# Kernel optimization log

Measured on AMD Instinct MI355X. Metric: run time of the kernel, lower is better.

## Reference

```python
import jax, jax.numpy as jnp
import numpy as np

# Constants from the torch module
S_DECAY = 0.95    # sentence_decay
P_DECAY = 0.99    # paragraph_decay
D_DECAY = 0.999   # document_decay
ALPHA = 0.1       # delta_update alpha for sentence/paragraph
DOC_ALPHA = 0.05  # delta_update alpha for document
BETA = 1.0
PARA_GROUP = 5    # sentences per paragraph
EPS = 1e-12       # F.normalize eps


def _normalize(x):
    # matches torch.nn.functional.normalize(x, dim=-1)
    return x / jnp.maximum(jnp.linalg.norm(x, axis=-1, keepdims=True), EPS)


def _delta_step(M, kn, v, alpha, beta):
    # M: [H, dk, dv]; kn: [dk] (already L2-normalized); v: [dv]
    # M_new = M @ (I - alpha * kn kn^T) + beta * kn v^T   (erase matrix is symmetric,
    # so the einsum 'hkv,hkj->hjv' form equals this rank-1 update -- no dk x dk matrix needed)
    kTM = jnp.einsum('k,hkv->hv', kn, M)                       # [H, dv]
    return M - alpha * kn[None, :, None] * kTM[:, None, :] \
             + beta * (kn[:, None] * v[None, :])[None, :, :]


def _scan_updates(M0, K, V, decay, alpha, beta):
    # Streaming delta-rule: per step, decay then erase/write.
    def step(M, kv):
        k, v = kv
        M = M * decay
        M = _delta_step(M, _normalize(k), v, alpha, beta)
        return M, None
    M, _ = jax.lax.scan(step, M0, (K, V))
    return M


def setup_inputs() -> dict:
    key = jax.random.key(0)
    ks = jax.random.split(key, 7)
    T, d_emb, d_k, d_v, H = 1000, 768, 256, 256, 8
    emb = jax.random.normal(ks[0], (T, d_emb), dtype=jnp.float32)
    q = jax.random.normal(ks[1], (d_k,), dtype=jnp.float32)
    W_k = jax.random.normal(ks[2], (d_emb, d_k), dtype=jnp.float32) * 0.02
    b_k = jax.random.normal(ks[3], (d_k,), dtype=jnp.float32) * 0.02
    W_v = jax.random.normal(ks[4], (d_emb, d_v), dtype=jnp.float32) * 0.02
    b_v = jax.random.normal(ks[5], (d_v,), dtype=jnp.float32) * 0.02
    M_sent0 = jnp.zeros((H, d_k, d_v), dtype=jnp.float32)
    M_para0 = jnp.zeros((H, d_k, d_v), dtype=jnp.float32)
    M_doc0 = jnp.zeros((H, d_k, d_v), dtype=jnp.float32)
    return {"emb": emb, "q": q, "W_k": W_k, "b_k": b_k, "W_v": W_v, "b_v": b_v,
            "M_sent0": M_sent0, "M_para0": M_para0, "M_doc0": M_doc0}


def reference(emb, q, W_k, b_k, W_v, b_v, M_sent0, M_para0, M_doc0):
    T, d_emb = emb.shape
    # Level 1: sentence memory -- one delta update per sentence embedding
    K = emb @ W_k + b_k            # [T, dk]
    V = emb @ W_v + b_v            # [T, dv]
    M_sent = _scan_updates(M_sent0, K, V, S_DECAY, ALPHA, BETA)
    # Level 2: paragraph memory -- mean of each group of 5 sentence embeddings
    para_emb = emb.reshape(T // PARA_GROUP, PARA_GROUP, d_emb).mean(axis=1)
    PK = para_emb @ W_k + b_k
    PV = para_emb @ W_v + b_v
    M_para = _scan_updates(M_para0, PK, PV, P_DECAY, ALPHA, BETA)
    # Level 3: document memory -- single update from paragraph-memory statistics
    doc_k = M_para.mean(axis=0).mean(axis=-1)   # [dk]
    doc_v = M_para.mean(axis=0).mean(axis=0)    # [dv]
    M_doc = M_doc0 * D_DECAY
    M_doc = _delta_step(M_doc, _normalize(doc_k), doc_v, DOC_ALPHA, BETA)
    # recall(q, level='all')
    qn = _normalize(q)
    def recall(M):
        return jnp.einsum('hkv,k->hv', M, qn).mean(axis=0)   # [dv]
    return 0.2 * recall(M_sent) + 0.3 * recall(M_para) + 0.5 * recall(M_doc)
```

## Files before the change

kernel.cpp:

```cpp
#include <hip/hip_runtime.h>
#include <hip/hip_bf16.h>

#define ALPHA   0.1f
#define S_DECAY 0.95f
#define P_DECAY 0.99f
#define D_EMB   768
#define DK      256

template<int ctrl, int row_mask>
__device__ __forceinline__ float dpp_add(float x) {
    int y = __builtin_amdgcn_update_dpp(0, __float_as_int(x), ctrl, row_mask, 0xF, true);
    return x + __int_as_float(y);
}

template<int N>
__device__ __forceinline__ void wave_allred_arr(float (&x)[N]) {
#pragma unroll
    for (int n = 0; n < N; ++n) x[n] = dpp_add<0xB1,  0xF>(x[n]);
#pragma unroll
    for (int n = 0; n < N; ++n) x[n] = dpp_add<0x4E,  0xF>(x[n]);
#pragma unroll
    for (int n = 0; n < N; ++n) x[n] = dpp_add<0x141, 0xF>(x[n]);
#pragma unroll
    for (int n = 0; n < N; ++n) x[n] = dpp_add<0x140, 0xF>(x[n]);
#pragma unroll
    for (int n = 0; n < N; ++n) x[n] = dpp_add<0x142, 0xA>(x[n]);
#pragma unroll
    for (int n = 0; n < N; ++n) x[n] = dpp_add<0x143, 0xC>(x[n]);
#pragma unroll
    for (int n = 0; n < N; ++n)
        x[n] = __int_as_float(__builtin_amdgcn_readlane(__float_as_int(x[n]), 63));
}

__device__ __forceinline__ float dot4v(const float4& a, const float4& b) {
    float t0 = a.x * b.x; t0 = fmaf(a.y, b.y, t0);
    float t1 = a.z * b.z; t1 = fmaf(a.w, b.w, t1);
    return t0 + t1;
}

__device__ __forceinline__ float rl(float x, int lane) {
    return __int_as_float(__builtin_amdgcn_readlane(__float_as_int(x), lane));
}

__global__ __launch_bounds__(256) void prep_kernel(
    const float* __restrict__ emb,
    const float* __restrict__ Wk, const float* __restrict__ bk,
    const float* __restrict__ Wv, const float* __restrict__ bv,
    float* __restrict__ K, float* __restrict__ V, float* __restrict__ USrev,
    float* __restrict__ out, int T)
{
    const int tid = threadIdx.x;
    const int bid = blockIdx.x;
    const int NBLK = (T / 4) * 2;
    if (bid >= NBLK) {
        const int PADS = ((T + 63) / 64) * 64;
        for (int i = tid; i < (PADS - T) * DK; i += 256) USrev[(size_t)T * DK + i] = 0.f;
        out[tid] = 0.f;
        return;
    }
    const int mat = bid & 1;
    const int r0  = (bid >> 1) * 4;

    __shared__ float se[4][D_EMB];
    __shared__ float s_red[4][4];

    const float4* emb4 = reinterpret_cast<const float4*>(emb);
#pragma unroll
    for (int r = 0; r < 4; ++r) {
        if (tid < D_EMB / 4)
            reinterpret_cast<float4*>(se[r])[tid] = emb4[(size_t)(r0 + r) * (D_EMB / 4) + tid];
    }
    __syncthreads();

    const float* Wp = mat ? Wv : Wk;
    const float* bp = mat ? bv : bk;
    const int j = tid;

    float a0 = 0.f, a1 = 0.f, a2 = 0.f, a3 = 0.f;
    float c0 = Wp[j],        c1 = Wp[j + DK],     c2 = Wp[j + 2*DK], c3 = Wp[j + 3*DK];
    float p0 = Wp[j + 4*DK], p1 = Wp[j + 5*DK],   p2 = Wp[j + 6*DK], p3 = Wp[j + 7*DK];

    for (int d = 0; d < D_EMB; d += 4) {
        int dn = d + 8; if (dn >= D_EMB) dn = 0;
        const float* wn = Wp + (size_t)dn * DK + j;
        float n0 = wn[0], n1 = wn[DK], n2 = wn[2*DK], n3 = wn[3*DK];

        float4 e0 = *reinterpret_cast<const float4*>(&se[0][d]);
        float4 e1 = *reinterpret_cast<const float4*>(&se[1][d]);
        float4 e2 = *reinterpret_cast<const float4*>(&se[2][d]);
        float4 e3 = *reinterpret_cast<const float4*>(&se[3][d]);

        a0 = fmaf(e0.x, c0, a0); a0 = fmaf(e0.y, c1, a0);
        a0 = fmaf(e0.z, c2, a0); a0 = fmaf(e0.w, c3, a0);
        a1 = fmaf(e1.x, c0, a1); a1 = fmaf(e1.y, c1, a1);
        a1 = fmaf(e1.z, c2, a1); a1 = fmaf(e1.w, c3, a1);
        a2 = fmaf(e2.x, c0, a2); a2 = fmaf(e2.y, c1, a2);
        a2 = fmaf(e2.z, c2, a2); a2 = fmaf(e2.w, c3, a2);
        a3 = fmaf(e3.x, c0, a3); a3 = fmaf(e3.y, c1, a3);
        a3 = fmaf(e3.z, c2, a3); a3 = fmaf(e3.w, c3, a3);

        c0 = p0; c1 = p1; c2 = p2; c3 = p3;
        p0 = n0; p1 = n1; p2 = n2; p3 = n3;
    }

    float bj = bp[j];
    float o0 = a0 + bj, o1 = a1 + bj, o2 = a2 + bj, o3 = a3 + bj;
    float* dst = mat ? V : K;
    dst[(size_t)(r0 + 0) * DK + j] = o0;
    dst[(size_t)(r0 + 1) * DK + j] = o1;
    dst[(size_t)(r0 + 2) * DK + j] = o2;
    dst[(size_t)(r0 + 3) * DK + j] = o3;

    if (mat == 0) {
        const int wave = tid >> 6, l = tid & 63;
        float red[4] = { o0*o0, o1*o1, o2*o2, o3*o3 };
        wave_allred_arr(red);
        if (l == 0) {
            s_red[wave][0] = red[0]; s_red[wave][1] = red[1];
            s_red[wave][2] = red[2]; s_red[wave][3] = red[3];
        }
        __syncthreads();
        float t0 = s_red[0][0] + s_red[1][0] + s_red[2][0] + s_red[3][0];
        float t1 = s_red[0][1] + s_red[1][1] + s_red[2][1] + s_red[3][1];
        float t2 = s_red[0][2] + s_red[1][2] + s_red[2][2] + s_red[3][2];
        float t3 = s_red[0][3] + s_red[1][3] + s_red[2][3] + s_red[3][3];
        USrev[(size_t)(T - 1 - (r0 + 0)) * DK + j] = o0 * (1.0f / fmaxf(sqrtf(t0), 1e-12f));
        USrev[(size_t)(T - 1 - (r0 + 1)) * DK + j] = o1 * (1.0f / fmaxf(sqrtf(t1), 1e-12f));
        USrev[(size_t)(T - 1 - (r0 + 2)) * DK + j] = o2 * (1.0f / fmaxf(sqrtf(t2), 1e-12f));
        USrev[(size_t)(T - 1 - (r0 + 3)) * DK + j] = o3 * (1.0f / fmaxf(sqrtf(t3), 1e-12f));
    }
}

#define SU_STRIDE 260
__global__ __launch_bounds__(512) void mid_kernel(
    const float* __restrict__ K, const float* __restrict__ V,
    const float* __restrict__ USrev,
    float* __restrict__ UPrev, float* __restrict__ UPfwd,
    float* __restrict__ PV, float* __restrict__ SVv,
    float* __restrict__ AinvT, float* __restrict__ F1, float* __restrict__ biasF,
    int P, int NCS, int NCP)
{
    __shared__ __align__(16) float sU[64 * SU_STRIDE];
    __shared__ __align__(16) float sA[64 * 65];
    __shared__ float s_pd[64];
    __shared__ float s_sv[64];
    __shared__ float4 s_f1w[4][64];
    float* sX = sU;

    const int tid = threadIdx.x, wv = tid >> 6, l = tid & 63;
    const int bid = blockIdx.x;
    int type, m;
    if (bid < NCS)            { type = 0; m = bid; }
    else if (bid < NCS + NCP) { type = 1; m = bid - NCS; }
    else                      { type = 2; m = bid - NCS - NCP; }

    if (type == 2) {
        if (tid < 64) s_pd[tid] = powf(P_DECAY, (float)tid);
        __syncthreads();
    }

    if (type == 0) {
        const float4* U4 = reinterpret_cast<const float4*>(USrev) + (size_t)m * 4096;
        for (int idx = tid; idx < 4096; idx += 512) {
            float4 t = U4[idx];
            int row = idx >> 6, c4 = (idx & 63) << 2;
            *reinterpret_cast<float4*>(&sU[row * SU_STRIDE + c4]) = t;
        }
    } else if (type == 1) {
        if (tid < 256) {
            const float4* K4 = reinterpret_cast<const float4*>(K);
            for (int ii = 0; ii < 16; ii += 2) {
                const int iA = wv * 16 + ii, iB = iA + 1;
                const int pA = P - 1 - (64 * m + iA);
                const int pB = P - 1 - (64 * m + iB);
                float4 ka[5], kb[5];
                if (pA >= 0) {
#pragma unroll
                    for (int s = 0; s < 5; ++s) ka[s] = K4[(size_t)(5 * pA + s) * 64 + l];
                }
                if (pB >= 0) {
#pragma unroll
                    for (int s = 0; s < 5; ++s) kb[s] = K4[(size_t)(5 * pB + s) * 64 + l];
                }
                {
                    float4 u = make_float4(0.f, 0.f, 0.f, 0.f);
                    if (pA >= 0) {
                        float4 pk = make_float4(0.f, 0.f, 0.f, 0.f);
#pragma unroll
                        for (int s = 0; s < 5; ++s) {
                            pk.x += ka[s].x; pk.y += ka[s].y; pk.z += ka[s].z; pk.w += ka[s].w;
                        }
                        pk.x *= 0.2f; pk.y *= 0.2f; pk.z *= 0.2f; pk.w *= 0.2f;
                        float red[1] = { dot4v(pk, pk) };
                        wave_allred_arr(red);
                        float inv = 1.0f / fmaxf(sqrtf(red[0]), 1e-12f);
                        u = make_float4(pk.x * inv, pk.y * inv, pk.z * inv, pk.w * inv);
                    }
                    *reinterpret_cast<float4*>(&sU[iA * SU_STRIDE + 4 * l]) = u;
                    reinterpret_cast<float4*>(UPrev)[(size_t)(64 * m + iA) * 64 + l] = u;
                }
                {
                    float4 u = make_float4(0.f, 0.f, 0.f, 0.f);
                    if (pB >= 0) {
                        float4 pk = make_float4(0.f, 0.f, 0.f, 0.f);
#pragma unroll
                        for (int s = 0; s < 5; ++s) {
                            pk.x += kb[s].x; pk.y += kb[s].y; pk.z += kb[s].z; pk.w += kb[s].w;
                        }
                        pk.x *= 0.2f; pk.y *= 0.2f; pk.z *= 0.2f; pk.w *= 0.2f;
                        float red[1] = { dot4v(pk, pk) };
                        wave_allred_arr(red);
                        float inv = 1.0f / fmaxf(sqrtf(red[0]), 1e-12f);
                        u = make_float4(pk.x * inv, pk.y * inv, pk.z * inv, pk.w * inv);
                    }
                    *reinterpret_cast<float4*>(&sU[iB * SU_STRIDE + 4 * l]) = u;
                    reinterpret_cast<float4*>(UPrev)[(size_t)(64 * m + iB) * 64 + l] = u;
                }
            }
        }
    } else {
        if (tid < 256) {
            const float4* K4 = reinterpret_cast<const float4*>(K);
            const float4* V4 = reinterpret_cast<const float4*>(V);
            float4 f1p = make_float4(0.f, 0.f, 0.f, 0.f);
            for (int ii = 0; ii < 16; ii += 2) {
                const int iA = wv * 16 + ii, iB = iA + 1;
                const int pA = 64 * m + iA, pB = 64 * m + iB;
                float4 ka[5], va[5], kb[5], vb[5];
                if (pA < P) {
#pragma unroll
                    for (int s = 0; s < 5; ++s) {
                        ka[s] = K4[(size_t)(5 * pA + s) * 64 + l];
                        va[s] = V4[(size_t)(5 * pA + s) * 64 + l];
                    }
                }
                if (pB < P) {
#pragma unroll
                    for (int s = 0; s < 5; ++s) {
                        kb[s] = K4[(size_t)(5 * pB + s) * 64 + l];
                        vb[s] = V4[(size_t)(5 * pB + s) * 64 + l];
                    }
                }
                {
                    float4 u = make_float4(0.f, 0.f, 0.f, 0.f);
                    float sv = 0.f;
                    if (pA < P) {
                        float4 pk = make_float4(0.f, 0.f, 0.f, 0.f);
                        float4 pv = make_float4(0.f, 0.f, 0.f, 0.f);
#pragma unroll
                        for (int s = 0; s < 5; ++s) {
                            pk.x += ka[s].x; pk.y += ka[s].y; pk.z += ka[s].z; pk.w += ka[s].w;
                            pv.x += va[s].x; pv.y += va[s].y; pv.z += va[s].z; pv.w += va[s].w;
                        }
                        pk.x *= 0.2f; pk.y *= 0.2f; pk.z *= 0.2f; pk.w *= 0.2f;
                        pv.x *= 0.2f; pv.y *= 0.2f; pv.z *= 0.2f; pv.w *= 0.2f;
                        reinterpret_cast<float4*>(PV)[(size_t)pA * 64 + l] = pv;
                        float red[2] = { dot4v(pk, pk), pv.x + pv.y + pv.z + pv.w };
                        wave_allred_arr(red);
                        float inv = 1.0f / fmaxf(sqrtf(red[0]), 1e-12f);
                        u = make_float4(pk.x * inv, pk.y * inv, pk.z * inv, pk.w * inv);
                        sv = red[1];
                    }
                    *reinterpret_cast<float4*>(&sU[iA * SU_STRIDE + 4 * l]) = u;
                    reinterpret_cast<float4*>(UPfwd)[(size_t)(64 * m + iA) * 64 + l] = u;
                    if (l == 0) { s_sv[iA] = sv; SVv[64 * m + iA] = sv; }
                    float f = s_pd[63 - iA] * sv;
                    f1p.x = fmaf(f, u.x, f1p.x); f1p.y = fmaf(f, u.y, f1p.y);
                    f1p.z = fmaf(f, u.z, f1p.z); f1p.w = fmaf(f, u.w, f1p.w);
                }
                {
                    float4 u = make_float4(0.f, 0.f, 0.f, 0.f);
                    float sv = 0.f;
                    if (pB < P) {
                        float4 pk = make_float4(0.f, 0.f, 0.f, 0.f);
                        float4 pv = make_float4(0.f, 0.f, 0.f, 0.f);
#pragma unroll
                        for (int s = 0; s < 5; ++s) {
                            pk.x += kb[s].x; pk.y += kb[s].y; pk.z += kb[s].z; pk.w += kb[s].w;
                            pv.x += vb[s].x; pv.y += vb[s].y; pv.z += vb[s].z; pv.w += vb[s].w;
                        }
                        pk.x *= 0.2f; pk.y *= 0.2f; pk.z *= 0.2f; pk.w *= 0.2f;
                        pv.x *= 0.2f; pv.y *= 0.2f; pv.z *= 0.2f; pv.w *= 0.2f;
                        reinterpret_cast<float4*>(PV)[(size_t)pB * 64 + l] = pv;
                        float red[2] = { dot4v(pk, pk), pv.x + pv.y + pv.z + pv.w };
                        wave_allred_arr(red);
                        float inv = 1.0f / fmaxf(sqrtf(red[0]), 1e-12f);
                        u = make_float4(pk.x * inv, pk.y * inv, pk.z * inv, pk.w * inv);
                        sv = red[1];
                    }
                    *reinterpret_cast<float4*>(&sU[iB * SU_STRIDE + 4 * l]) = u;
                    reinterpret_cast<float4*>(UPfwd)[(size_t)(64 * m + iB) * 64 + l] = u;
                    if (l == 0) { s_sv[iB] = sv; SVv[64 * m + iB] = sv; }
                    float f = s_pd[63 - iB] * sv;
                    f1p.x = fmaf(f, u.x, f1p.x); f1p.y = fmaf(f, u.y, f1p.y);
                    f1p.z = fmaf(f, u.z, f1p.z); f1p.w = fmaf(f, u.w, f1p.w);
                }
            }
            s_f1w[wv][l] = f1p;
        }
    }
    __syncthreads();

    if (type == 2 && wv == 0) {
        float4 a = s_f1w[0][l], b = s_f1w[1][l], c = s_f1w[2][l], d = s_f1w[3][l];
        float4 tot = make_float4(a.x+b.x+c.x+d.x, a.y+b.y+c.y+d.y,
                                 a.z+b.z+c.z+d.z, a.w+b.w+c.w+d.w);
        reinterpret_cast<float4*>(F1)[(size_t)m * 64 + l] = tot;
    }

    {
        const int i0 = (tid & 31) * 2;
        const int j0 = (tid >> 5) * 4;
        float g[2][4];
#pragma unroll
        for (int r = 0; r < 2; ++r)
#pragma unroll
            for (int c = 0; c < 4; ++c) g[r][c] = 0.f;
#pragma unroll 4
        for (int k4 = 0; k4 < 64; ++k4) {
            float4 A0 = *reinterpret_cast<const float4*>(&sU[(i0    ) * SU_STRIDE + 4*k4]);
            float4 A1 = *reinterpret_cast<const float4*>(&sU[(i0 + 1) * SU_STRIDE + 4*k4]);
            float4 B0 = *reinterpret_cast<const float4*>(&sU[(j0    ) * SU_STRIDE + 4*k4]);
            float4 B1 = *reinterpret_cast<const float4*>(&sU[(j0 + 1) * SU_STRIDE + 4*k4]);
            float4 B2 = *reinterpret_cast<const float4*>(&sU[(j0 + 2) * SU_STRIDE + 4*k4]);
            float4 B3 = *reinterpret_cast<const float4*>(&sU[(j0 + 3) * SU_STRIDE + 4*k4]);
            g[0][0] += dot4v(A0, B0); g[0][1] += dot4v(A0, B1);
            g[0][2] += dot4v(A0, B2); g[0][3] += dot4v(A0, B3);
            g[1][0] += dot4v(A1, B0); g[1][1] += dot4v(A1, B1);
            g[1][2] += dot4v(A1, B2); g[1][3] += dot4v(A1, B3);
        }
#pragma unroll
        for (int r = 0; r < 2; ++r)
#pragma unroll
            for (int c = 0; c < 4; ++c) {
                int gi = i0 + r, gj = j0 + c;
                float val = 0.f;
                if (gj < gi) {
                    val = ALPHA * g[r][c];
                    if (type == 2) val *= s_pd[gi - gj];
                }
                sA[gi * 65 + gj] = val;
            }
    }
    __syncthreads();

    if (type == 2 && wv == 0) {
        float dotb = 0.f;
#pragma unroll
        for (int jj = 0; jj < 64; ++jj)
            dotb = fmaf(sA[l * 65 + jj], s_sv[jj], dotb);
        biasF[m * 64 + l] = dotb * (1.0f / ALPHA);
    }

    {
        const int base = (wv & 3) * 16;
        float x[16];
#pragma unroll
        for (int r = 0; r < 16; ++r) x[r] = (base + r == l && wv < 4) ? 1.f : 0.f;
        for (int s = 0; s < 4; ++s) {
            if (wv == s) {
#pragma unroll
                for (int i = 1; i < 16; ++i)
#pragma unroll
                    for (int jj = 0; jj < 16; ++jj)
                        if (jj < i)
                            x[i] = fmaf(-sA[(base + i) * 65 + (base + jj)], x[jj], x[i]);
#pragma unroll
                for (int r = 0; r < 16; ++r) sX[(base + r) * 65 + l] = x[r];
            }
            __syncthreads();
            if (wv > s && wv < 4) {
#pragma unroll
                for (int i = 0; i < 16; ++i) {
                    float xi = sX[(s * 16 + i) * 65 + l];
#pragma unroll
                    for (int r = 0; r < 16; ++r)
                        x[r] = fmaf(-sA[(base + r) * 65 + (s * 16 + i)], xi, x[r]);
                }
            }
        }
    }
    __syncthreads();

    float* dstA = AinvT + (size_t)bid * 4096;
    for (int idx = tid; idx < 4096; idx += 512) {
        int jcol = idx >> 6, irow = idx & 63;
        dstA[idx] = sX[irow * 65 + jcol];
    }
}

__global__ __launch_bounds__(512) void accum2_kernel(
    const float* __restrict__ V, const float* __restrict__ PV,
    const float* __restrict__ USrev, const float* __restrict__ UPrev,
    const float* __restrict__ UPfwd, const float* __restrict__ AinvT,
    const float* __restrict__ F1, const float* __restrict__ biasF,
    const float* __restrict__ q,
    float* __restrict__ out, int T, int P, int NCS, int NCP)
{
    __shared__ float s_cp[8][64];
    __shared__ float4 s_part[8][64];
    __shared__ float s_powd[65];
    __shared__ float s_b[64];
    __shared__ float s_cpa[4][64];
    __shared__ float wc[64];
    __shared__ float s_gs[1];

    const int b = blockIdx.x, tid = threadIdx.x;
    const int wave = tid >> 6, l = tid & 63, wb = wave * 8;

    if (tid <= 64) s_powd[tid] = powf(P_DECAY, (float)tid);

    float4 q4 = reinterpret_cast<const float4*>(q)[l];
    float qs[1] = { dot4v(q4, q4) };
    wave_allred_arr(qs);
    float qinv = 1.0f / fmaxf(sqrtf(qs[0]), 1e-12f);
    float4 qn = make_float4(q4.x * qinv, q4.y * qinv, q4.z * qinv, q4.w * qinv);
    __syncthreads();

    int ci, chunk, realN; const float* src; float decay;
    if (b < NCS)              { ci = b;             chunk = b;        src = V;  decay = S_DECAY; realN = T; }
    else if (b < NCS + NCP)   { ci = b - NCS;       chunk = NCS + ci; src = PV; decay = P_DECAY; realN = P; }
    else                      { ci = b - NCS - NCP; chunk = NCS + ci; src = PV; decay = P_DECAY; realN = P; }

    {
        const float4* U4; const float* Xb; float4 w1;
        if (b < NCS) {
            U4 = reinterpret_cast<const float4*>(USrev); Xb = AinvT; w1 = qn;
        } else if (b < NCS + NCP) {
            U4 = reinterpret_cast<const float4*>(UPrev); Xb = AinvT + (size_t)NCS * 4096; w1 = qn;
        } else {
            U4 = reinterpret_cast<const float4*>(UPrev); Xb = AinvT + (size_t)NCS * 4096;
            w1 = make_float4(1.f, 1.f, 1.f, 1.f);
        }
        for (int m = 0; m <= ci; ++m) {
            float4 curU[8];
#pragma unroll
            for (int r = 0; r < 8; ++r)
                curU[r] = U4[(size_t)m * 4096 + (size_t)(wb + r) * 64 + l];
            float d[8];
#pragma unroll
            for (int r = 0; r < 8; ++r) d[r] = dot4v(curU[r], w1);
            wave_allred_arr(d);
            if (m == ci) {
                if (l == 0) {
#pragma unroll
                    for (int r = 0; r < 8; ++r) s_b[wb + r] = d[r];
                }
                break;
            }
            float curX[8];
#pragma unroll
            for (int r = 0; r < 8; ++r)
                curX[r] = Xb[(size_t)m * 4096 + (size_t)(wb + r) * 64 + l];
            float cp = 0.f;
#pragma unroll
            for (int r = 0; r < 8; ++r) cp = fmaf(curX[r], d[r], cp);
            s_cp[wave][l] = cp;
            __syncthreads();
            float cl = 0.f;
#pragma unroll
            for (int w = 0; w < 8; ++w) cl += s_cp[w][l];
            float4 part = make_float4(0.f, 0.f, 0.f, 0.f);
#pragma unroll
            for (int r = 0; r < 8; ++r) {
                float cw = rl(cl, wb + r);
                part.x = fmaf(cw, curU[r].x, part.x); part.y = fmaf(cw, curU[r].y, part.y);
                part.z = fmaf(cw, curU[r].z, part.z); part.w = fmaf(cw, curU[r].w, part.w);
            }
            s_part[wave][l] = part;
            __syncthreads();
            float4 s = make_float4(0.f, 0.f, 0.f, 0.f);
#pragma unroll
            for (int w = 0; w < 8; ++w) {
                float4 p = s_part[w][l];
                s.x += p.x; s.y += p.y; s.z += p.z; s.w += p.w;
            }
            w1.x = fmaf(-ALPHA, s.x, w1.x); w1.y = fmaf(-ALPHA, s.y, w1.y);
            w1.z = fmaf(-ALPHA, s.z, w1.z); w1.w = fmaf(-ALPHA, s.w, w1.w);
        }
    }
    __syncthreads();

    if (b >= NCS + NCP) {
        float4 y = make_float4(0.f, 0.f, 0.f, 0.f);
        const float4* Uf4 = reinterpret_cast<const float4*>(UPfwd);
        for (int mm = 0; mm < NCP; ++mm) {
            float4 cU[8]; float cX[8];
#pragma unroll
            for (int r = 0; r < 8; ++r) {
                cU[r] = Uf4[(size_t)mm * 4096 + (size_t)(wb + r) * 64 + l];
                cX[r] = AinvT[(size_t)(NCS + NCP + mm) * 4096 + (size_t)(wb + r) * 64 + l];
            }
            float biasr[8];
#pragma unroll
            for (int r = 0; r < 8; ++r) biasr[r] = biasF[mm * 64 + wb + r];
            float4 f1 = reinterpret_cast<const float4*>(F1)[(size_t)mm * 64 + l];
            float d[8];
#pragma unroll
            for (int r = 0; r < 8; ++r) d[r] = dot4v(cU[r], y);
            wave_allred_arr(d);
#pragma unroll
            for (int r = 0; r < 8; ++r)
                d[r] = fmaf(s_powd[wb + r + 1], d[r], biasr[r]);
            float cp = 0.f;
#pragma unroll
            for (int r = 0; r < 8; ++r) cp = fmaf(cX[r], d[r], cp);
            s_cp[wave][l] = cp;
            __syncthreads();
            float cl = 0.f;
#pragma unroll
            for (int w = 0; w < 8; ++w) cl += s_cp[w][l];
            float4 part = make_float4(0.f, 0.f, 0.f, 0.f);
#pragma unroll
            for (int r = 0; r < 8; ++r) {
                float cw = s_powd[63 - (wb + r)] * rl(cl, wb + r);
                part.x = fmaf(cw, cU[r].x, part.x); part.y = fmaf(cw, cU[r].y, part.y);
                part.z = fmaf(cw, cU[r].z, part.z); part.w = fmaf(cw, cU[r].w, part.w);
            }
            s_part[wave][l] = part;
            __syncthreads();
            float4 s = make_float4(0.f, 0.f, 0.f, 0.f);
#pragma unroll
            for (int w = 0; w < 8; ++w) {
                float4 p = s_part[w][l];
                s.x += p.x; s.y += p.y; s.z += p.z; s.w += p.w;
            }
            float d64 = s_powd[64];
            y.x = fmaf(d64, y.x, fmaf(-ALPHA, s.x, f1.x));
            y.y = fmaf(d64, y.y, fmaf(-ALPHA, s.y, f1.y));
            y.z = fmaf(d64, y.z, fmaf(-ALPHA, s.z, f1.z));
            y.w = fmaf(d64, y.w, fmaf(-ALPHA, s.w, f1.w));
        }
        float fin[2] = { dot4v(y, y), dot4v(qn, y) };
        wave_allred_arr(fin);
        if (tid == 0) s_gs[0] = fin[1] / fmaxf(sqrtf(fin[0]), 2.56e-10f);
        __syncthreads();
    }

    if (tid < 256) {
        const int part = tid >> 6, k = tid & 63;
        const float* Xc = AinvT + (size_t)chunk * 4096;
        float cp = 0.f;
#pragma unroll
        for (int jj = 0; jj < 16; ++jj) {
            int j = part * 16 + jj;
            cp = fmaf(Xc[j * 64 + k], s_b[j], cp);
        }
        s_cpa[part][k] = cp;
    }
    __syncthreads();
    if (tid < 64) {
        float c = s_cpa[0][tid] + s_cpa[1][tid] + s_cpa[2][tid] + s_cpa[3][tid];
        wc[tid] = powf(decay, (float)(ci * 64 + tid)) * c;
    }
    __syncthreads();
    if (tid < 256) {
        const int k = tid;
        float acc = 0.f;
        for (int ii = 0; ii < 64; ++ii) {
            int i = ci * 64 + ii;
            if (i < realN)
                acc = fmaf(wc[ii], src[(size_t)(realN - 1 - i) * DK + k], acc);
        }
        float wlev;
        if (b < NCS)            wlev = 0.2f;
        else if (b < NCS + NCP) wlev = 0.3f;
        else                    wlev = (0.5f / 256.0f) * s_gs[0];
        atomicAdd(&out[k], wlev * acc);
    }
}

extern "C" void kernel_launch(void* const* d_in, const int* in_sizes, int n_in,
                              void* d_out, int out_size, void* d_ws, size_t ws_size,
                              hipStream_t stream) {
    const float* emb = (const float*)d_in[0];
    const float* q   = (const float*)d_in[1];
    const float* Wk  = (const float*)d_in[2];
    const float* bk  = (const float*)d_in[3];
    const float* Wv  = (const float*)d_in[4];
    const float* bv  = (const float*)d_in[5];

    const int T = in_sizes[0] / D_EMB;
    const int P = T / 5;
    const int NCS  = (T + 63) / 64;
    const int NCP  = (P + 63) / 64;
    const int PADS = NCS * 64;
    const int PADP = NCP * 64;
    const int NCH  = NCS + 2 * NCP;

    float* ws    = (float*)d_ws;
    float* K     = ws;
    float* V     = K     + (size_t)T * DK;
    float* PV    = V     + (size_t)T * DK;
    float* USrev = PV    + (size_t)PADP * DK;
    float* UPrev = USrev + (size_t)PADS * DK;
    float* UPfwd = UPrev + (size_t)PADP * DK;
    float* SVv   = UPfwd + (size_t)PADP * DK;
    float* AinvT = SVv   + PADP;
    float* F1    = AinvT + (size_t)NCH * 4096;
    float* biasF = F1    + (size_t)NCP * 256;

    prep_kernel<<<(T / 4) * 2 + 1, 256, 0, stream>>>(emb, Wk, bk, Wv, bv,
                                                     K, V, USrev, (float*)d_out, T);
    mid_kernel<<<NCH, 512, 0, stream>>>(K, V, USrev, UPrev, UPfwd, PV, SVv,
                                        AinvT, F1, biasF, P, NCS, NCP);
    accum2_kernel<<<NCH, 512, 0, stream>>>(V, PV, USrev, UPrev, UPfwd, AinvT,
                                           F1, biasF, q, (float*)d_out, T, P, NCS, NCP);
}
```

Baseline: 173.4 us.

## Run serial chunk recurrence in one wave and prefetch source rows into LDS

The sequential per-chunk recurrence in accum2_kernel now runs entirely inside wave 0, which handles all 64 rows itself and so needs no block-wide barriers per chunk. Meanwhile waves 4-7 stage the block's 64x256 source rows into a 64KB shared buffer, and threads 0-255 prefetch their AinvT slice into registers. The aim is to remove two __syncthreads per iteration and overlap the final accumulation's global loads with the serial phase. The cost is 8x more serial work per wave, heavy register pressure from the 64-entry dfull arrays, and lower occupancy from the large LDS allocation.

New measurement: 305.0 us. 75.9% more time.

```diff
diff --git a/kernel.cpp b/kernel.cpp
--- a/kernel.cpp
+++ b/kernel.cpp
@@ -397,8 +397,7 @@
     const float* __restrict__ q,
     float* __restrict__ out, int T, int P, int NCS, int NCP)
 {
-    __shared__ float s_cp[8][64];
-    __shared__ float4 s_part[8][64];
+    __shared__ float s_src[64 * 256];
     __shared__ float s_powd[65];
     __shared__ float s_b[64];
     __shared__ float s_cpa[4][64];
@@ -406,7 +405,7 @@
     __shared__ float s_gs[1];
 
     const int b = blockIdx.x, tid = threadIdx.x;
-    const int wave = tid >> 6, l = tid & 63, wb = wave * 8;
+    const int wave = tid >> 6, l = tid & 63;
 
     if (tid <= 64) s_powd[tid] = powf(P_DECAY, (float)tid);
 
@@ -422,129 +421,167 @@
     else if (b < NCS + NCP)   { ci = b - NCS;       chunk = NCS + ci; src = PV; decay = P_DECAY; realN = P; }
     else                      { ci = b - NCS - NCP; chunk = NCS + ci; src = PV; decay = P_DECAY; realN = P; }
 
-    {
-        const float4* U4; const float* Xb; float4 w1;
-        if (b < NCS) {
-            U4 = reinterpret_cast<const float4*>(USrev); Xb = AinvT; w1 = qn;
-        } else if (b < NCS + NCP) {
-            U4 = reinterpret_cast<const float4*>(UPrev); Xb = AinvT + (size_t)NCS * 4096; w1 = qn;
-        } else {
-            U4 = reinterpret_cast<const float4*>(UPrev); Xb = AinvT + (size_t)NCS * 4096;
-            w1 = make_float4(1.f, 1.f, 1.f, 1.f);
-        }
-        for (int m = 0; m <= ci; ++m) {
-            float4 curU[8];
-#pragma unroll
-            for (int r = 0; r < 8; ++r)
-                curU[r] = U4[(size_t)m * 4096 + (size_t)(wb + r) * 64 + l];
-            float d[8];
-#pragma unroll
-            for (int r = 0; r < 8; ++r) d[r] = dot4v(curU[r], w1);
-            wave_allred_arr(d);
-            if (m == ci) {
-                if (l == 0) {
-#pragma unroll
-                    for (int r = 0; r < 8; ++r) s_b[wb + r] = d[r];
-                }
-                break;
-            }
-            float curX[8];
-#pragma unroll
-            for (int r = 0; r < 8; ++r)
-                curX[r] = Xb[(size_t)m * 4096 + (size_t)(wb + r) * 64 + l];
-            float cp = 0.f;
-#pragma unroll
-            for (int r = 0; r < 8; ++r) cp = fmaf(curX[r], d[r], cp);
-            s_cp[wave][l] = cp;
-            __syncthreads();
-            float cl = 0.f;
-#pragma unroll
-            for (int w = 0; w < 8; ++w) cl += s_cp[w][l];
-            float4 part = make_float4(0.f, 0.f, 0.f, 0.f);
-#pragma unroll
-            for (int r = 0; r < 8; ++r) {
-                float cw = rl(cl, wb + r);
-                part.x = fmaf(cw, curU[r].x, part.x); part.y = fmaf(cw, curU[r].y, part.y);
-                part.z = fmaf(cw, curU[r].z, part.z); part.w = fmaf(cw, curU[r].w, part.w);
-            }
-            s_part[wave][l] = part;
-            __syncthreads();
-            float4 s = make_float4(0.f, 0.f, 0.f, 0.f);
-#pragma unroll
-            for (int w = 0; w < 8; ++w) {
-                float4 p = s_part[w][l];
-                s.x += p.x; s.y += p.y; s.z += p.z; s.w += p.w;
-            }
-            w1.x = fmaf(-ALPHA, s.x, w1.x); w1.y = fmaf(-ALPHA, s.y, w1.y);
-            w1.z = fmaf(-ALPHA, s.z, w1.z); w1.w = fmaf(-ALPHA, s.w, w1.w);
-        }
-    }
-    __syncthreads();
-
-    if (b >= NCS + NCP) {
-        float4 y = make_float4(0.f, 0.f, 0.f, 0.f);
-        const float4* Uf4 = reinterpret_cast<const float4*>(UPfwd);
-        for (int mm = 0; mm < NCP; ++mm) {
-            float4 cU[8]; float cX[8];
-#pragma unroll
-            for (int r = 0; r < 8; ++r) {
-                cU[r] = Uf4[(size_t)mm * 4096 + (size_t)(wb + r) * 64 + l];
-                cX[r] = AinvT[(size_t)(NCS + NCP + mm) * 4096 + (size_t)(wb + r) * 64 + l];
-            }
-            float biasr[8];
-#pragma unroll
-            for (int r = 0; r < 8; ++r) biasr[r] = biasF[mm * 64 + wb + r];
-            float4 f1 = reinterpret_cast<const float4*>(F1)[(size_t)mm * 64 + l];
-            float d[8];
-#pragma unroll
-            for (int r = 0; r < 8; ++r) d[r] = dot4v(cU[r], y);
-            wave_allred_arr(d);
-#pragma unroll
-            for (int r = 0; r < 8; ++r)
-                d[r] = fmaf(s_powd[wb + r + 1], d[r], biasr[r]);
-            float cp = 0.f;
-#pragma unroll
-            for (int r = 0; r < 8; ++r) cp = fmaf(cX[r], d[r], cp);
-            s_cp[wave][l] = cp;
-            __syncthreads();
-            float cl = 0.f;
-#pragma unroll
-            for (int w = 0; w < 8; ++w) cl += s_cp[w][l];
-            float4 part = make_float4(0.f, 0.f, 0.f, 0.f);
-#pragma unroll
-            for (int r = 0; r < 8; ++r) {
-                float cw = s_powd[63 - (wb + r)] * rl(cl, wb + r);
-                part.x = fmaf(cw, cU[r].x, part.x); part.y = fmaf(cw, cU[r].y, part.y);
-                part.z = fmaf(cw, cU[r].z, part.z); part.w = fmaf(cw, cU[r].w, part.w);
-            }
-            s_part[wave][l] = part;
-            __syncthreads();
-            float4 s = make_float4(0.f, 0.f, 0.f, 0.f);
-#pragma unroll
-            for (int w = 0; w < 8; ++w) {
-                float4 p = s_part[w][l];
-                s.x += p.x; s.y += p.y; s.z += p.z; s.w += p.w;
-            }
-            float d64 = s_powd[64];
-            y.x = fmaf(d64, y.x, fmaf(-ALPHA, s.x, f1.x));
-            y.y = fmaf(d64, y.y, fmaf(-ALPHA, s.y, f1.y));
-            y.z = fmaf(d64, y.z, fmaf(-ALPHA, s.z, f1.z));
-            y.w = fmaf(d64, y.w, fmaf(-ALPHA, s.w, f1.w));
-        }
-        float fin[2] = { dot4v(y, y), dot4v(qn, y) };
-        wave_allred_arr(fin);
-        if (tid == 0) s_gs[0] = fin[1] / fmaxf(sqrtf(fin[0]), 2.56e-10f);
-        __syncthreads();
-    }
-
+    float xr[16];
     if (tid < 256) {
         const int part = tid >> 6, k = tid & 63;
         const float* Xc = AinvT + (size_t)chunk * 4096;
+#pragma unroll
+        for (int jj = 0; jj < 16; ++jj)
+            xr[jj] = Xc[(part * 16 + jj) * 64 + k];
+    }
+
+    if (wave == 0) {
+        {
+            const float4* U4; const float* Xb; float4 w1;
+            if (b < NCS) {
+                U4 = reinterpret_cast<const float4*>(USrev); Xb = AinvT; w1 = qn;
+            } else if (b < NCS + NCP) {
+                U4 = reinterpret_cast<const float4*>(UPrev); Xb = AinvT + (size_t)NCS * 4096; w1 = qn;
+            } else {
+                U4 = reinterpret_cast<const float4*>(UPrev); Xb = AinvT + (size_t)NCS * 4096;
+                w1 = make_float4(1.f, 1.f, 1.f, 1.f);
+            }
+            for (int m = 0; m <= ci; ++m) {
+                const size_t base = (size_t)m * 4096;
+                float dfull[64];
+#pragma unroll
+                for (int g = 0; g < 8; ++g) {
+                    float4 u[8];
+#pragma unroll
+                    for (int r = 0; r < 8; ++r)
+                        u[r] = U4[base + (size_t)(g * 8 + r) * 64 + l];
+                    float dd[8];
+#pragma unroll
+                    for (int r = 0; r < 8; ++r) dd[r] = dot4v(u[r], w1);
+                    wave_allred_arr(dd);
+#pragma unroll
+                    for (int r = 0; r < 8; ++r) dfull[g * 8 + r] = dd[r];
+                }
+                if (m == ci) {
+                    if (l == 0) {
+#pragma unroll
+                        for (int j = 0; j < 64; ++j) s_b[j] = dfull[j];
+                    }
+                    break;
+                }
+                float cl = 0.f;
+#pragma unroll
+                for (int g = 0; g < 8; ++g) {
+                    float xg[8];
+#pragma unroll
+                    for (int r = 0; r < 8; ++r)
+                        xg[r] = Xb[base + (size_t)(g * 8 + r) * 64 + l];
+                    float cp = 0.f;
+#pragma unroll
+                    for (int r = 0; r < 8; ++r) cp = fmaf(xg[r], dfull[g * 8 + r], cp);
+                    cl += cp;
+                }
+                float4 s = make_float4(0.f, 0.f, 0.f, 0.f);
+#pragma unroll
+                for (int g = 0; g < 8; ++g) {
+                    float4 u[8];
+#pragma unroll
+                    for (int r = 0; r < 8; ++r)
+                        u[r] = U4[base + (size_t)(g * 8 + r) * 64 + l];
+                    float4 part = make_float4(0.f, 0.f, 0.f, 0.f);
+#pragma unroll
+                    for (int r = 0; r < 8; ++r) {
+                        float cw = rl(cl, g * 8 + r);
+                        part.x = fmaf(cw, u[r].x, part.x); part.y = fmaf(cw, u[r].y, part.y);
+                        part.z = fmaf(cw, u[r].z, part.z); part.w = fmaf(cw, u[r].w, part.w);
+                    }
+                    s.x += part.x; s.y += part.y; s.z += part.z; s.w += part.w;
+                }
+                w1.x = fmaf(-ALPHA, s.x, w1.x); w1.y = fmaf(-ALPHA, s.y, w1.y);
+                w1.z = fmaf(-ALPHA, s.z, w1.z); w1.w = fmaf(-ALPHA, s.w, w1.w);
+            }
+        }
+
+        if (b >= NCS + NCP) {
+            float4 y = make_float4(0.f, 0.f, 0.f, 0.f);
+            const float4* Uf4 = reinterpret_cast<const float4*>(UPfwd);
+            for (int mm = 0; mm < NCP; ++mm) {
+                const size_t ubase = (size_t)mm * 4096;
+                const float* Xf = AinvT + (size_t)(NCS + NCP + mm) * 4096;
+                float bl = biasF[mm * 64 + l];
+                float4 f1 = reinterpret_cast<const float4*>(F1)[(size_t)mm * 64 + l];
+                float dfull[64];
+#pragma unroll
+                for (int g = 0; g < 8; ++g) {
+                    float4 u[8];
+#pragma unroll
+                    for (int r = 0; r < 8; ++r)
+                        u[r] = Uf4[ubase + (size_t)(g * 8 + r) * 64 + l];
+                    float dd[8];
+#pragma unroll
+                    for (int r = 0; r < 8; ++r) dd[r] = dot4v(u[r], y);
+                    wave_allred_arr(dd);
+#pragma unroll
+                    for (int r = 0; r < 8; ++r) {
+                        const int j = g * 8 + r;
+                        dfull[j] = fmaf(s_powd[j + 1], dd[r], rl(bl, j));
+                    }
+                }
+                float cl = 0.f;
+#pragma unroll
+                for (int g = 0; g < 8; ++g) {
+                    float xg[8];
+#pragma unroll
+                    for (int r = 0; r < 8; ++r)
+                        xg[r] = Xf[(size_t)(g * 8 + r) * 64 + l];
+                    float cp = 0.f;
+#pragma unroll
+                    for (int r = 0; r < 8; ++r) cp = fmaf(xg[r], dfull[g * 8 + r], cp);
+                    cl += cp;
+                }
+                float4 s = make_float4(0.f, 0.f, 0.f, 0.f);
+#pragma unroll
+                for (int g = 0; g < 8; ++g) {
+                    float4 u[8];
+#pragma unroll
+                    for (int r = 0; r < 8; ++r)
+                        u[r] = Uf4[ubase + (size_t)(g * 8 + r) * 64 + l];
+                    float4 part = make_float4(0.f, 0.f, 0.f, 0.f);
+#pragma unroll
+                    for (int r = 0; r < 8; ++r) {
+                        const int j = g * 8 + r;
+                        float cw = s_powd[63 - j] * rl(cl, j);
+                        part.x = fmaf(cw, u[r].x, part.x); part.y = fmaf(cw, u[r].y, part.y);
+                        part.z = fmaf(cw, u[r].z, part.z); part.w = fmaf(cw, u[r].w, part.w);
+                    }
+                    s.x += part.x; s.y += part.y; s.z += part.z; s.w += part.w;
+                }
+                float d64 = s_powd[64];
+                y.x = fmaf(d64, y.x, fmaf(-ALPHA, s.x, f1.x));
+                y.y = fmaf(d64, y.y, fmaf(-ALPHA, s.y, f1.y));
+                y.z = fmaf(d64, y.z, fmaf(-ALPHA, s.z, f1.z));
+                y.w = fmaf(d64, y.w, fmaf(-ALPHA, s.w, f1.w));
+            }
+            float fin[2] = { dot4v(y, y), dot4v(qn, y) };
+            wave_allred_arr(fin);
+            if (l == 0) s_gs[0] = fin[1] / fmaxf(sqrtf(fin[0]), 2.56e-10f);
+        }
+    } else if (tid >= 256) {
+        const float4* src4 = reinterpret_cast<const float4*>(src);
+        float4* s_src4 = reinterpret_cast<float4*>(s_src);
+#pragma unroll
+        for (int t = 0; t < 16; ++t) {
+            int idx = (tid - 256) + 256 * t;
+            int row = idx >> 6, c4 = idx & 63;
+            int i = ci * 64 + row;
+            if (i < realN)
+                s_src4[row * 64 + c4] = src4[(size_t)(realN - 1 - i) * 64 + c4];
+        }
+    }
+    __syncthreads();
+
+    if (tid < 256) {
+        const int part = tid >> 6, k = tid & 63;
         float cp = 0.f;
 #pragma unroll
         for (int jj = 0; jj < 16; ++jj) {
             int j = part * 16 + jj;
-            cp = fmaf(Xc[j * 64 + k], s_b[j], cp);
+            cp = fmaf(xr[jj], s_b[j], cp);
         }
         s_cpa[part][k] = cp;
     }
@@ -560,7 +597,7 @@
         for (int ii = 0; ii < 64; ++ii) {
             int i = ci * 64 + ii;
             if (i < realN)
-                acc = fmaf(wc[ii], src[(size_t)(realN - 1 - i) * DK + k], acc);
+                acc = fmaf(wc[ii], s_src[ii * 256 + k], acc);
         }
         float wlev;
         if (b < NCS)            wlev = 0.2f;
```
